# Performance work log

Measured on AMD Instinct MI355X. Metric: run time of the kernel, lower is better.

Reference implementation:

```python
import jax, jax.numpy as jnp
import numpy as np

N, E = 50000, 500000
DH, DL = 13, 128          # handcrafted / learned node feature dims
OH, OL = 32, 96           # node-encoder output dims; node_dim D = OH+OL
D = OH + OL               # 128
EIN = (DH + DL) + 1 + 3 * D + 1  # 527, forced by concat in forward
H = 256                   # MLP hidden width
HC = 64                   # classifier hidden width
EPS = 1e-8


def _mlp(x, W1, b1, W2, b2):
    # 2-layer MLP with ReLU, matching repo MLP(fc_dims=[H, out])
    return jax.nn.relu(x @ W1 + b1) @ W2 + b2


def _cosine(a, b):
    # torch.nn.CosineSimilarity(dim=1, eps=1e-8)
    na = jnp.maximum(jnp.linalg.norm(a, axis=-1), EPS)
    nb = jnp.maximum(jnp.linalg.norm(b, axis=-1), EPS)
    return jnp.sum(a * b, axis=-1) / (na * nb)


def _lin(key, fan_in, fan_out):
    kW, kb = jax.random.split(key)
    s = 1.0 / np.sqrt(fan_in)
    return (jax.random.uniform(kW, (fan_in, fan_out), jnp.float32, -s, s),
            jax.random.uniform(kb, (fan_out,), jnp.float32, -s, s))


def setup_inputs() -> dict:
    key = jax.random.key(0)
    ks = jax.random.split(key, 16)
    x1 = jax.random.normal(ks[0], (N, DH), jnp.float32)
    x2 = jax.random.normal(ks[1], (N, DL), jnp.float32)
    edge_index = jax.random.randint(ks[2], (2, E), 0, N, jnp.int64)
    Wh1, bh1 = _lin(ks[3], DH, H);   Wh2, bh2 = _lin(ks[4], H, OH)
    Wl1, bl1 = _lin(ks[5], DL, H);   Wl2, bl2 = _lin(ks[6], H, OL)
    We1, be1 = _lin(ks[7], EIN, H);  We2, be2 = _lin(ks[8], H, D)
    Wmsg, bmsg = _lin(ks[9], 2 * D, D)
    Wnode, bnode = _lin(ks[10], 2 * D, D)
    Wmp1, bmp1 = _lin(ks[11], 3 * D, H); Wmp2, bmp2 = _lin(ks[12], H, D)
    Wc1, bc1 = _lin(ks[13], D, HC);  Wc2, bc2 = _lin(ks[14], HC, 1)
    return dict(x1=x1, x2=x2, edge_index=edge_index,
                Wh1=Wh1, bh1=bh1, Wh2=Wh2, bh2=bh2,
                Wl1=Wl1, bl1=bl1, Wl2=Wl2, bl2=bl2,
                We1=We1, be1=be1, We2=We2, be2=be2,
                Wmsg=Wmsg, bmsg=bmsg, Wnode=Wnode, bnode=bnode,
                Wmp1=Wmp1, bmp1=bmp1, Wmp2=Wmp2, bmp2=bmp2,
                Wc1=Wc1, bc1=bc1, Wc2=Wc2, bc2=bc2)


def reference(x1, x2, edge_index,
              Wh1, bh1, Wh2, bh2,
              Wl1, bl1, Wl2, bl2,
              We1, be1, We2, be2,
              Wmsg, bmsg, Wnode, bnode,
              Wmp1, bmp1, Wmp2, bmp2,
              Wc1, bc1, Wc2, bc2):
    src, trg = edge_index[0], edge_index[1]
    # raw-feature edge descriptors
    x_init = jnp.concatenate((x1, x2), axis=-1)            # [N, 141]
    xi_s, xi_t = x_init[src], x_init[trg]                  # gathers [E, 141]
    sim1 = _cosine(xi_s, xi_t)                             # [E]
    abs_init = jnp.abs(xi_s - xi_t)                        # [E, 141]
    # node encoders
    h1 = _mlp(x1, Wh1, bh1, Wh2, bh2)                      # [N, 32]
    h2 = _mlp(x2, Wl1, bl1, Wl2, bl2)                      # [N, 96]
    x = jnp.concatenate((h1, h2), axis=-1)                 # [N, 128]
    xs, xt = x[src], x[trg]                                # [E, 128]
    sim2 = _cosine(xs, xt)                                 # [E]
    edge_feat_in = jnp.concatenate(
        (abs_init, sim1[:, None], xs, xt, jnp.abs(xs - xt), sim2[:, None]),
        axis=-1)                                           # [E, 527]
    e = _mlp(edge_feat_in, We1, be1, We2, be2)             # [E, 128]
    # edge MPNN round: edge->node aggregation, node update, edge update
    msg = jax.nn.relu(jnp.concatenate((xs, e), axis=-1) @ Wmsg + bmsg)  # [E, 128]
    agg = jax.ops.segment_sum(msg, trg, num_segments=N)    # [N, 128]
    xn = jax.nn.relu(jnp.concatenate((x, agg), axis=-1) @ Wnode + bnode)  # [N, 128]
    e_mp = _mlp(jnp.concatenate((xn[src], xn[trg], e), axis=-1),
                Wmp1, bmp1, Wmp2, bmp2)                    # [E, 128]
    pred = _mlp(e_mp, Wc1, bc1, Wc2, bc2)                  # [E, 1]
    return jnp.squeeze(pred, axis=-1)                      # [E]
```

## Files before the change

kernel.cpp:

```cpp
#include <hip/hip_runtime.h>
#include <hip/hip_bf16.h>
#include <hip/hip_fp16.h>


using fp16 = __half;
typedef _Float16 h16;
typedef _Float16 f16x8 __attribute__((ext_vector_type(8)));
typedef float f32x4 __attribute__((ext_vector_type(4)));

#define NN 50000
#define EE 500000
#define EPSC 1e-8f

__device__ __forceinline__ float reluf(float v){ return v > 0.f ? v : 0.f; }

#define OFF_E1   0
#define OFF_E2   139264
#define OFF_MSG  172032
#define OFF_NODE 204800
#define OFF_MP1  237568
#define OFF_MP2  335872
#define OFF_C1   368640
#define OFF_N1   376832
#define OFF_N2   458752
#define WT_TOTAL 524288
#define BF_TOTAL 640

__global__ __launch_bounds__(256) void k_prep(
    const float* __restrict__ We1, const float* __restrict__ We2,
    const float* __restrict__ Wmsg, const float* __restrict__ Wnode,
    const float* __restrict__ Wmp1, const float* __restrict__ Wmp2,
    const float* __restrict__ Wc1,
    const float* __restrict__ Wh1, const float* __restrict__ Wl1,
    const float* __restrict__ Wh2, const float* __restrict__ Wl2,
    const float* __restrict__ bh1, const float* __restrict__ bl1,
    const float* __restrict__ bh2, const float* __restrict__ bl2,
    h16* __restrict__ WT, float* __restrict__ BF)
{
  int idx = blockIdx.x * 256 + threadIdx.x;
  if (idx >= WT_TOTAL) {
    const int b = idx - WT_TOTAL;
    if (b < 512) BF[b] = (b < 256) ? bh1[b] : bl1[b - 256];
    else if (b < BF_TOTAL) {
      const int c = b - 512;
      BF[b] = (c < 32) ? bh2[c] : bl2[c - 32];
    }
    return;
  }
  h16 v;
  if (idx < OFF_E2) {
    const int L = idx, n = L / 544, k = L % 544;
    int r;
    if      (k < 128) r = 142 + k;
    else if (k < 256) r = 270 + (k - 128);
    else if (k < 384) r = 398 + (k - 256);
    else if (k < 512) r = 13 + (k - 384);
    else if (k < 525) r = k - 512;
    else if (k == 528) r = 141;
    else if (k == 529) r = 526;
    else r = -1;
    v = (h16)((r >= 0) ? We1[r * 256 + n] : 0.f);
  } else if (idx < OFF_MSG) {
    const int L = idx - OFF_E2, n = L >> 8, k = L & 255;
    v = (h16)We2[k * 128 + n];
  } else if (idx < OFF_NODE) {
    const int L = idx - OFF_MSG, n = L >> 8, k = L & 255;
    const int ko = (k < 128) ? (128 + k) : (k - 128);
    v = (h16)Wmsg[ko * 128 + n];
  } else if (idx < OFF_MP1) {
    const int L = idx - OFF_NODE, n = L >> 8, k = L & 255;
    v = (h16)Wnode[k * 128 + n];
  } else if (idx < OFF_MP2) {
    const int L = idx - OFF_MP1, n = L / 384, k = L % 384;
    v = (h16)Wmp1[k * 256 + n];
  } else if (idx < OFF_C1) {
    const int L = idx - OFF_MP2, n = L >> 8, k = L & 255;
    v = (h16)Wmp2[k * 128 + n];
  } else if (idx < OFF_N1) {
    const int L = idx - OFF_C1, n = L >> 7, k = L & 127;
    v = (h16)Wc1[k * 64 + n];
  } else if (idx < OFF_N2) {
    const int L = idx - OFF_N1, n = L / 160, k = L % 160;
    float f = 0.f;
    if (n < 256) { if (k < 13) f = Wh1[k * 256 + n]; }
    else { if (k >= 16 && k < 144) f = Wl1[(k - 16) * 256 + (n - 256)]; }
    v = (h16)f;
  } else {
    const int L = idx - OFF_N2, n = L >> 9, k = L & 511;
    float f = 0.f;
    if (n < 32) { if (k < 256) f = Wh2[k * 32 + n]; }
    else { if (k >= 256) f = Wl2[(k - 256) * 96 + (n - 32)]; }
    v = (h16)f;
  }
  WT[idx] = v;
}

__global__ __launch_bounds__(256) void k_cvt(
    const float* __restrict__ x1, const float* __restrict__ x2,
    h16* __restrict__ X1P, h16* __restrict__ X2H)
{
  const int idx = blockIdx.x * 256 + threadIdx.x;
  if (idx < NN * 16) {
    const int nn = idx >> 4, j = idx & 15;
    X1P[idx] = (h16)((j < 13) ? x1[nn * 13 + j] : 0.f);
  }
  const int i2 = idx - NN * 16;
  if (i2 >= 0 && i2 < NN * 128) X2H[i2] = (h16)x2[i2];
}

__global__ __launch_bounds__(256) void k_hist(
    const int* __restrict__ ei, int* __restrict__ CNT)
{
  const int e = blockIdx.x * 256 + threadIdx.x;
  if (e < EE) atomicAdd(&CNT[ei[EE + e]], 1);
}

__global__ __launch_bounds__(1024) void k_scan(
    const int* __restrict__ CNT, int* __restrict__ OFF)
{
  __shared__ int sdata[1024];
  __shared__ int scarry;
  const int tid = threadIdx.x;
  if (tid == 0) { scarry = 0; OFF[0] = 0; }
  __syncthreads();
  for (int base = 0; base < NN; base += 1024) {
    const int i = base + tid;
    sdata[tid] = (i < NN) ? CNT[i] : 0;
    __syncthreads();
    for (int off = 1; off < 1024; off <<= 1) {
      const int x = (tid >= off) ? sdata[tid - off] : 0;
      __syncthreads();
      sdata[tid] += x;
      __syncthreads();
    }
    const int carry = scarry;
    if (i < NN) OFF[i + 1] = sdata[tid] + carry;
    __syncthreads();
    if (tid == 0) scarry = carry + sdata[1023];
    __syncthreads();
  }
}

__global__ __launch_bounds__(256) void k_scatter(
    const int* __restrict__ ei, const int* __restrict__ OFF,
    int* __restrict__ POS, int* __restrict__ ES,
    int* __restrict__ ET, int* __restrict__ OID)
{
  const int e = blockIdx.x * 256 + threadIdx.x;
  if (e >= EE) return;
  const int t = ei[EE + e];
  const int p = atomicAdd(&POS[t], 1);
  const int idx = OFF[t] + p;
  ES[idx] = ei[e];
  ET[idx] = t;
  OID[idx] = e;
}

template<int ROWS, int UDIM, int KP, int LDA, int WAVES, bool RELU,
         bool ENDSYNC, typename F>
__device__ __forceinline__ void mfma_gemm(const h16* sA,
    const h16* __restrict__ WT, const float* __restrict__ bias, F emit)
{
  constexpr int RT = ROWS / 16;
  constexpr int NPW0 = UDIM / WAVES;
  constexpr int NPW = (NPW0 < 16) ? 16 : NPW0;
  constexpr int NT = NPW / 16;
  constexpr int NSTEPS = KP / 32;
  constexpr int CH0 = (NT >= 4) ? 2 : 4;
  constexpr int CHUNK = (NSTEPS < CH0) ? NSTEPS : CH0;
  constexpr int NCH = (NSTEPS + CHUNK - 1) / CHUNK;
  const int tid = threadIdx.x;
  const int wave = tid >> 6;
  const int lane = tid & 63;
  const int m = lane & 15;
  const int quad = lane >> 4;
  const int n0 = wave * NPW;
  const bool active = (n0 < UDIM);

  f32x4 acc[RT][NT];
#pragma unroll
  for (int r = 0; r < RT; ++r)
#pragma unroll
    for (int j = 0; j < NT; ++j) acc[r][j] = (f32x4){0.f, 0.f, 0.f, 0.f};
  float bb[NT];

  if (active) {
    const h16* wbase = &WT[(size_t)(n0 + m) * KP + quad * 8];
#pragma unroll
    for (int j = 0; j < NT; ++j) bb[j] = bias[n0 + j * 16 + m];

    f16x8 breg[2][CHUNK][NT];
#pragma unroll
    for (int s = 0; s < CHUNK; ++s)
      if (s < NSTEPS)
#pragma unroll
        for (int j = 0; j < NT; ++j)
          breg[0][s][j] = *(const f16x8*)&wbase[(size_t)j * 16 * KP + s * 32];
    asm volatile("" ::: "memory");

#pragma unroll
    for (int c = 0; c < NCH; ++c) {
      if (c + 1 < NCH) {
#pragma unroll
        for (int s = 0; s < CHUNK; ++s) {
          const int st = (c + 1) * CHUNK + s;
          if (st < NSTEPS)
#pragma unroll
            for (int j = 0; j < NT; ++j)
              breg[(c + 1) & 1][s][j] =
                  *(const f16x8*)&wbase[(size_t)j * 16 * KP + st * 32];
        }
      }
#pragma unroll
      for (int s = 0; s < CHUNK; ++s) {
        const int st = c * CHUNK + s;
        if (st < NSTEPS) {
          const int k0 = st * 32;
#pragma unroll
          for (int r = 0; r < RT; ++r) {
            const f16x8 af = *(const f16x8*)&sA[(r * 16 + m) * LDA + k0 + quad * 8];
#pragma unroll
            for (int j = 0; j < NT; ++j)
              acc[r][j] = __builtin_amdgcn_mfma_f32_16x16x32_f16(af, breg[c & 1][s][j], acc[r][j], 0, 0, 0);
          }
        }
      }
      asm volatile("" ::: "memory");
    }
  }
  __syncthreads();
  if (active) {
#pragma unroll
    for (int j = 0; j < NT; ++j) {
      const int col = n0 + j * 16 + m;
#pragma unroll
      for (int r = 0; r < RT; ++r)
#pragma unroll
        for (int g = 0; g < 4; ++g) {
          const int row = r * 16 + quad * 4 + g;
          float v = acc[r][j][g] + bb[j];
          if (RELU) v = reluf(v);
          emit(row, col, v);
        }
    }
  }
  if (ENDSYNC) __syncthreads();
}

__global__ __launch_bounds__(512, 4) void k_nenc(
    const h16* __restrict__ X1P, const h16* __restrict__ X2H,
    const h16* __restrict__ WT, const float* __restrict__ BF,
    h16* __restrict__ XH)
{
  __shared__ __align__(16) h16 sA[32 * 168];
  __shared__ __align__(16) h16 sH[32 * 520];
  const int tid = threadIdx.x;
  const int n0 = blockIdx.x * 32;
  const int remn = NN - n0;
  const int cnt = remn < 32 ? remn : 32;
  const int n = tid >> 4;
  const int q = tid & 15;

  if (n < cnt) {
    const int node = n0 + n;
    if (q < 2)
      *(f16x8*)&sA[n * 168 + q * 8] = *(const f16x8*)&X1P[node * 16 + q * 8];
    else if (q < 4)
      *(f16x8*)&sA[n * 168 + 144 + (q - 2) * 8] = (f16x8){};
    *(f16x8*)&sA[n * 168 + 16 + q * 8] =
        *(const f16x8*)&X2H[(size_t)node * 128 + q * 8];
  }
  __syncthreads();

  mfma_gemm<32, 512, 160, 168, 8, true, true>(sA, WT + OFF_N1, BF,
      [&](int row, int col, float v) { sH[row * 520 + col] = (h16)v; });
  mfma_gemm<32, 128, 512, 520, 8, false, false>(sH, WT + OFF_N2, BF + 512,
      [&](int row, int col, float v) {
        if (row < cnt) XH[(size_t)(n0 + row) * 128 + col] = (h16)v;
      });
}

__global__ __launch_bounds__(512, 4) void k_edge_mlp(
    const h16* __restrict__ X1P, const h16* __restrict__ X2H,
    const int* __restrict__ ES, const int* __restrict__ ET,
    const h16* __restrict__ XH, const h16* __restrict__ WT,
    const float* __restrict__ be1, const float* __restrict__ be2,
    const float* __restrict__ bmsg,
    h16* __restrict__ EB, float* __restrict__ AGG)
{
  __shared__ __align__(16) h16 sFeat[64 * 568];
  __shared__ int strg[64];
  const int tid = threadIdx.x;
  const long e0 = (long)blockIdx.x * 64;
  const long rem = (long)EE - e0;
  const int cnt = rem < 64 ? (int)rem : 64;
  const int n = tid >> 3;
  const int q = tid & 7;
  h16* Arow = &sFeat[n * 568];
  f16x8 xsv0 = {}, xsv1 = {};

  if (n < cnt) {
    const int s = ES[e0 + n];
    const int t = ET[e0 + n];
    if (q == 0) strg[n] = t;
    float ds = 0.f, ns = 0.f, nt = 0.f;
    if (q < 2) {
      const f16x8 a = *(const f16x8*)&X1P[s * 16 + q * 8];
      const f16x8 b = *(const f16x8*)&X1P[t * 16 + q * 8];
      f16x8 d;
#pragma unroll
      for (int i = 0; i < 8; ++i) {
        const float av = (float)a[i], bv = (float)b[i];
        ds += av * bv; ns += av * av; nt += bv * bv;
        d[i] = (h16)fabsf(av - bv);
      }
      *(f16x8*)&Arow[512 + q * 8] = d;
    }
#pragma unroll
    for (int c = 0; c < 2; ++c) {
      const f16x8 a = *(const f16x8*)&X2H[(size_t)s * 128 + q * 16 + c * 8];
      const f16x8 b = *(const f16x8*)&X2H[(size_t)t * 128 + q * 16 + c * 8];
      f16x8 d;
#pragma unroll
      for (int i = 0; i < 8; ++i) {
        const float av = (float)a[i], bv = (float)b[i];
        ds += av * bv; ns += av * av; nt += bv * bv;
        d[i] = (h16)fabsf(av - bv);
      }
      *(f16x8*)&Arow[384 + q * 16 + c * 8] = d;
    }
    ds += __shfl_xor(ds, 1); ds += __shfl_xor(ds, 2); ds += __shfl_xor(ds, 4);
    ns += __shfl_xor(ns, 1); ns += __shfl_xor(ns, 2); ns += __shfl_xor(ns, 4);
    nt += __shfl_xor(nt, 1); nt += __shfl_xor(nt, 2); nt += __shfl_xor(nt, 4);
    if (q == 0)
      Arow[528] = (h16)(ds / (fmaxf(sqrtf(ns), EPSC) * fmaxf(sqrtf(nt), EPSC)));

    float ds2 = 0.f, ns2 = 0.f, nt2 = 0.f;
#pragma unroll
    for (int c = 0; c < 2; ++c) {
      const f16x8 a = *(const f16x8*)&XH[(size_t)s * 128 + q * 16 + c * 8];
      const f16x8 b = *(const f16x8*)&XH[(size_t)t * 128 + q * 16 + c * 8];
      if (c == 0) xsv0 = a; else xsv1 = a;
      f16x8 d;
#pragma unroll
      for (int i = 0; i < 8; ++i) {
        const float av = (float)a[i], bv = (float)b[i];
        ds2 += av * bv; ns2 += av * av; nt2 += bv * bv;
        d[i] = (h16)fabsf(av - bv);
      }
      *(f16x8*)&Arow[q * 16 + c * 8]       = a;
      *(f16x8*)&Arow[128 + q * 16 + c * 8] = b;
      *(f16x8*)&Arow[256 + q * 16 + c * 8] = d;
    }
    ds2 += __shfl_xor(ds2, 1); ds2 += __shfl_xor(ds2, 2); ds2 += __shfl_xor(ds2, 4);
    ns2 += __shfl_xor(ns2, 1); ns2 += __shfl_xor(ns2, 2); ns2 += __shfl_xor(ns2, 4);
    nt2 += __shfl_xor(nt2, 1); nt2 += __shfl_xor(nt2, 2); nt2 += __shfl_xor(nt2, 4);
    if (q == 0)
      Arow[529] = (h16)(ds2 / (fmaxf(sqrtf(ns2), EPSC) * fmaxf(sqrtf(nt2), EPSC)));
    for (int j = 530 + q; j < 544; j += 8) Arow[j] = (h16)0.f;
  } else {
    if (q == 0) strg[n] = 0;
    for (int j8 = q; j8 < 71; j8 += 8) *(f16x8*)&Arow[j8 * 8] = (f16x8){};
  }
  __syncthreads();

  h16* sHid = sFeat;
  mfma_gemm<64, 256, 544, 568, 8, true, true>(sFeat, WT + OFF_E1, be1,
      [&](int row, int col, float v) { sHid[row * 264 + col] = (h16)v; });
  mfma_gemm<64, 128, 256, 264, 8, false, false>(sHid, WT + OFF_E2, be2,
      [&](int row, int col, float v) {
        const h16 vh = (h16)v;
        if (row < cnt) EB[(size_t)(e0 + row) * 128 + col] = vh;
        sHid[row * 264 + col] = vh;
      });
  *(f16x8*)&sFeat[n * 264 + 128 + q * 16]     = xsv0;
  *(f16x8*)&sFeat[n * 264 + 128 + q * 16 + 8] = xsv1;
  __syncthreads();
  mfma_gemm<64, 128, 256, 264, 8, true, true>(sFeat, WT + OFF_MSG, bmsg,
      [&](int row, int col, float v) {
        *(float*)((char*)sFeat + row * 528 + col * 4) = v;
      });
  {
    const int c = tid & 127;
    const int g = tid >> 7;
    const int r0 = g * 16;
    if (r0 < cnt) {
      const int rend = (r0 + 16 < cnt) ? r0 + 16 : cnt;
      float acc = 0.f;
      int cur = strg[r0];
      for (int r = r0; r < rend; ++r) {
        const int t = strg[r];
        if (t != cur) {
          atomicAdd(&AGG[(size_t)cur * 128 + c], acc);
          acc = 0.f; cur = t;
        }
        acc += *(const float*)((const char*)sFeat + r * 528 + c * 4);
      }
      atomicAdd(&AGG[(size_t)cur * 128 + c], acc);
    }
  }
}

__global__ __launch_bounds__(256, 4) void k_node_update(
    const h16* __restrict__ XH, const float* __restrict__ AGG,
    const h16* __restrict__ WT, const float* __restrict__ bnode,
    h16* __restrict__ XNH)
{
  __shared__ __align__(16) h16 sA[64 * 264];
  const int tid = threadIdx.x;
  const int n0 = blockIdx.x * 64;
  const int remn = NN - n0;
  const int cnt = remn < 64 ? remn : 64;
  const int n = tid >> 2;
  const int q = tid & 3;

  if (n < cnt) {
    const f16x8* xr = (const f16x8*)&XH[(size_t)(n0 + n) * 128];
    const float4* ar = (const float4*)&AGG[(size_t)(n0 + n) * 128];
    for (int j8 = q; j8 < 16; j8 += 4)
      *(f16x8*)&sA[n * 264 + j8 * 8] = xr[j8];
    for (int j4 = q; j4 < 32; j4 += 4) {
      const float4 b = ar[j4];
      h16* p1 = &sA[n * 264 + 128 + j4 * 4];
      p1[0] = (h16)b.x; p1[1] = (h16)b.y; p1[2] = (h16)b.z; p1[3] = (h16)b.w;
    }
  } else {
    for (int j = q; j < 256; j += 4) sA[n * 264 + j] = (h16)0.f;
  }
  __syncthreads();

  mfma_gemm<64, 128, 256, 264, 4, true, false>(sA, WT + OFF_NODE, bnode,
      [&](int row, int col, float v) {
        if (row < cnt) XNH[(size_t)(n0 + row) * 128 + col] = (h16)v;
      });
}

__global__ __launch_bounds__(512, 4) void k_empl(
    const int* __restrict__ ES, const int* __restrict__ ET,
    const int* __restrict__ OID, const h16* __restrict__ XNH,
    const h16* __restrict__ EB, const h16* __restrict__ WT,
    const float* __restrict__ bmp1, const float* __restrict__ bmp2,
    const float* __restrict__ bc1,
    const float* __restrict__ Wc2, const float* __restrict__ bc2,
    float* __restrict__ out)
{
  __shared__ __align__(16) h16 sF[64 * 392];
  const int tid = threadIdx.x;
  const long e0 = (long)blockIdx.x * 64;
  const long rem = (long)EE - e0;
  const int cnt = rem < 64 ? (int)rem : 64;
  const int n = tid >> 3;
  const int q = tid & 7;

  if (n < cnt) {
    const int s = ES[e0 + n];
    const int t = ET[e0 + n];
    const f16x8* xsr = (const f16x8*)&XNH[(size_t)s * 128];
    const f16x8* xtr = (const f16x8*)&XNH[(size_t)t * 128];
    const f16x8* ebr = (const f16x8*)&EB[(size_t)(e0 + n) * 128];
#pragma unroll
    for (int j8 = q; j8 < 16; j8 += 8) {
      *(f16x8*)&sF[n * 392 + j8 * 8]       = xsr[j8];
      *(f16x8*)&sF[n * 392 + 128 + j8 * 8] = xtr[j8];
      *(f16x8*)&sF[n * 392 + 256 + j8 * 8] = ebr[j8];
    }
  } else {
    for (int j8 = q; j8 < 49; j8 += 8) *(f16x8*)&sF[n * 392 + j8 * 8] = (f16x8){};
  }
  __syncthreads();

  h16*  sH2 = sF;
  h16*  sE  = sF;
  float* sHC = (float*)((char*)sF + 17408);
  mfma_gemm<64, 256, 384, 392, 8, true, true>(sF, WT + OFF_MP1, bmp1,
      [&](int row, int col, float v) { sH2[row * 264 + col] = (h16)v; });
  mfma_gemm<64, 128, 256, 264, 8, false, true>(sH2, WT + OFF_MP2, bmp2,
      [&](int row, int col, float v) { sE[row * 136 + col] = (h16)v; });
  mfma_gemm<64, 64, 128, 136, 8, true, true>(sE, WT + OFF_C1, bc1,
      [&](int row, int col, float v) { sHC[row * 65 + col] = v; });
  if (tid < cnt) {
    float acc = bc2[0];
    for (int k = 0; k < 64; ++k) acc += sHC[tid * 65 + k] * Wc2[k];
    out[OID[e0 + tid]] = acc;
  }
}

extern "C" void kernel_launch(void* const* d_in, const int* in_sizes, int n_in,
                              void* d_out, int out_size, void* d_ws, size_t ws_size,
                              hipStream_t stream)
{
  const float* x1  = (const float*)d_in[0];
  const float* x2  = (const float*)d_in[1];
  const int*   ei  = (const int*)d_in[2];
  const float* Wh1 = (const float*)d_in[3],  *bh1 = (const float*)d_in[4];
  const float* Wh2 = (const float*)d_in[5],  *bh2 = (const float*)d_in[6];
  const float* Wl1 = (const float*)d_in[7],  *bl1 = (const float*)d_in[8];
  const float* Wl2 = (const float*)d_in[9],  *bl2 = (const float*)d_in[10];
  const float* We1 = (const float*)d_in[11], *be1 = (const float*)d_in[12];
  const float* We2 = (const float*)d_in[13], *be2 = (const float*)d_in[14];
  const float* Wmsg = (const float*)d_in[15], *bmsg = (const float*)d_in[16];
  const float* Wnode = (const float*)d_in[17], *bnode = (const float*)d_in[18];
  const float* Wmp1 = (const float*)d_in[19], *bmp1 = (const float*)d_in[20];
  const float* Wmp2 = (const float*)d_in[21], *bmp2 = (const float*)d_in[22];
  const float* Wc1 = (const float*)d_in[23], *bc1 = (const float*)d_in[24];
  const float* Wc2 = (const float*)d_in[25], *bc2 = (const float*)d_in[26];
  float* out = (float*)d_out;

  float* AGG = (float*)d_ws;
  h16*   EB  = (h16*)(AGG + (size_t)NN * 128);
  h16*   WT  = EB + (size_t)EE * 128;
  h16*   XH  = WT + WT_TOTAL;
  h16*   XNH = XH + (size_t)NN * 128;
  h16*   X1P = XNH + (size_t)NN * 128;
  h16*   X2H = X1P + (size_t)NN * 16;
  float* BF  = (float*)(X2H + (size_t)NN * 128);
  int*   CNT = (int*)(BF + BF_TOTAL);
  int*   POS = CNT + NN;
  int*   OFF = POS + NN;
  int*   ES  = OFF + (NN + 1);
  int*   ET  = ES + EE;
  int*   OID = ET + EE;

  k_prep<<<(WT_TOTAL + BF_TOTAL + 255) / 256, 256, 0, stream>>>(
      We1, We2, Wmsg, Wnode, Wmp1, Wmp2, Wc1,
      Wh1, Wl1, Wh2, Wl2, bh1, bl1, bh2, bl2, WT, BF);
  k_cvt<<<(NN * 16 + NN * 128 + 255) / 256, 256, 0, stream>>>(x1, x2, X1P, X2H);
  hipMemsetAsync(AGG, 0, (size_t)NN * 128 * sizeof(float), stream);
  hipMemsetAsync(CNT, 0, (size_t)2 * NN * sizeof(int), stream);
  k_hist<<<(EE + 255) / 256, 256, 0, stream>>>(ei, CNT);
  k_scan<<<1, 1024, 0, stream>>>(CNT, OFF);
  k_scatter<<<(EE + 255) / 256, 256, 0, stream>>>(ei, OFF, POS, ES, ET, OID);
  k_nenc<<<(NN + 31) / 32, 512, 0, stream>>>(X1P, X2H, WT, BF, XH);
  k_edge_mlp<<<7813, 512, 0, stream>>>(X1P, X2H, ES, ET, XH, WT,
                                       be1, be2, bmsg, EB, AGG);
  k_node_update<<<782, 256, 0, stream>>>(XH, AGG, WT, bnode, XNH);
  k_empl<<<7813, 512, 0, stream>>>(ES, ET, OID, XNH, EB, WT, bmp1, bmp2, bc1,
                                   Wc2, bc2, out);
}
```

Before: 951.3 us.

## Parallelize CSR scan, fuse histogram into convert, use fdot2 for cosine features

Replaces the single-block serial prefix scan over 50k node counts with a two-level multi-block scan, so this step is no longer a one-workgroup bottleneck. The in-degree histogram is folded into the input-conversion kernel to save a launch. The edge-feature kernel now computes its dot products and norms with packed fp16 dot2 instructions and takes absolute differences with a sign-bit mask, reducing per-element conversion work. The dot products now take fp16 inputs with fp32 accumulation, and the absolute differences are computed in fp16 rather than fp32, which may change rounding slightly.

```diff
diff --git a/kernel.cpp b/kernel.cpp
--- a/kernel.cpp
+++ b/kernel.cpp
@@ -6,13 +6,35 @@
 using fp16 = __half;
 typedef _Float16 h16;
 typedef _Float16 f16x8 __attribute__((ext_vector_type(8)));
+typedef _Float16 h16x2 __attribute__((ext_vector_type(2)));
+typedef short s16x8 __attribute__((ext_vector_type(8)));
 typedef float f32x4 __attribute__((ext_vector_type(4)));
 
 #define NN 50000
 #define EE 500000
 #define EPSC 1e-8f
+#define SCAN_B 196
 
 __device__ __forceinline__ float reluf(float v){ return v > 0.f ? v : 0.f; }
+
+__device__ __forceinline__ float dot8(const f16x8 a, const f16x8 b, float acc)
+{
+#pragma unroll
+  for (int i = 0; i < 4; ++i) {
+    const h16x2 av = {a[2 * i], a[2 * i + 1]};
+    const h16x2 bv = {b[2 * i], b[2 * i + 1]};
+    acc = __builtin_amdgcn_fdot2(av, bv, acc, false);
+  }
+  return acc;
+}
+
+__device__ __forceinline__ f16x8 absdiff8(const f16x8 a, const f16x8 b)
+{
+  const f16x8 d = a - b;
+  s16x8 di = __builtin_bit_cast(s16x8, d);
+  di &= (short)0x7fff;
+  return __builtin_bit_cast(f16x8, di);
+}
 
 #define OFF_E1   0
 #define OFF_E2   139264
@@ -97,9 +119,11 @@
 
 __global__ __launch_bounds__(256) void k_cvt(
     const float* __restrict__ x1, const float* __restrict__ x2,
-    h16* __restrict__ X1P, h16* __restrict__ X2H)
+    const int* __restrict__ ei,
+    h16* __restrict__ X1P, h16* __restrict__ X2H, int* __restrict__ CNT)
 {
   const int idx = blockIdx.x * 256 + threadIdx.x;
+  if (idx < EE) atomicAdd(&CNT[ei[EE + idx]], 1);
   if (idx < NN * 16) {
     const int nn = idx >> 4, j = idx & 15;
     X1P[idx] = (h16)((j < 13) ? x1[nn * 13 + j] : 0.f);
@@ -108,49 +132,52 @@
   if (i2 >= 0 && i2 < NN * 128) X2H[i2] = (h16)x2[i2];
 }
 
-__global__ __launch_bounds__(256) void k_hist(
-    const int* __restrict__ ei, int* __restrict__ CNT)
-{
-  const int e = blockIdx.x * 256 + threadIdx.x;
-  if (e < EE) atomicAdd(&CNT[ei[EE + e]], 1);
-}
-
-__global__ __launch_bounds__(1024) void k_scan(
-    const int* __restrict__ CNT, int* __restrict__ OFF)
-{
-  __shared__ int sdata[1024];
-  __shared__ int scarry;
-  const int tid = threadIdx.x;
-  if (tid == 0) { scarry = 0; OFF[0] = 0; }
-  __syncthreads();
-  for (int base = 0; base < NN; base += 1024) {
-    const int i = base + tid;
-    sdata[tid] = (i < NN) ? CNT[i] : 0;
+__global__ __launch_bounds__(256) void k_scanA(
+    const int* __restrict__ CNT, int* __restrict__ TEX, int* __restrict__ BS)
+{
+  __shared__ int sd[256];
+  const int tid = threadIdx.x;
+  const int i = blockIdx.x * 256 + tid;
+  const int v = (i < NN) ? CNT[i] : 0;
+  sd[tid] = v;
+  __syncthreads();
+  for (int off = 1; off < 256; off <<= 1) {
+    const int x = (tid >= off) ? sd[tid - off] : 0;
     __syncthreads();
-    for (int off = 1; off < 1024; off <<= 1) {
-      const int x = (tid >= off) ? sdata[tid - off] : 0;
-      __syncthreads();
-      sdata[tid] += x;
-      __syncthreads();
-    }
-    const int carry = scarry;
-    if (i < NN) OFF[i + 1] = sdata[tid] + carry;
+    sd[tid] += x;
     __syncthreads();
-    if (tid == 0) scarry = carry + sdata[1023];
+  }
+  if (i < NN) TEX[i] = sd[tid] - v;
+  if (tid == 255) BS[blockIdx.x] = sd[255];
+}
+
+__global__ __launch_bounds__(256) void k_scanB(
+    const int* __restrict__ BS, int* __restrict__ BSSE)
+{
+  __shared__ int sd[256];
+  const int tid = threadIdx.x;
+  const int v = (tid < SCAN_B) ? BS[tid] : 0;
+  sd[tid] = v;
+  __syncthreads();
+  for (int off = 1; off < 256; off <<= 1) {
+    const int x = (tid >= off) ? sd[tid - off] : 0;
     __syncthreads();
-  }
+    sd[tid] += x;
+    __syncthreads();
+  }
+  if (tid < SCAN_B) BSSE[tid] = sd[tid] - v;
 }
 
 __global__ __launch_bounds__(256) void k_scatter(
-    const int* __restrict__ ei, const int* __restrict__ OFF,
-    int* __restrict__ POS, int* __restrict__ ES,
-    int* __restrict__ ET, int* __restrict__ OID)
+    const int* __restrict__ ei, const int* __restrict__ TEX,
+    const int* __restrict__ BSSE, int* __restrict__ POS,
+    int* __restrict__ ES, int* __restrict__ ET, int* __restrict__ OID)
 {
   const int e = blockIdx.x * 256 + threadIdx.x;
   if (e >= EE) return;
   const int t = ei[EE + e];
   const int p = atomicAdd(&POS[t], 1);
-  const int idx = OFF[t] + p;
+  const int idx = BSSE[t >> 8] + TEX[t] + p;
   ES[idx] = ei[e];
   ET[idx] = t;
   OID[idx] = e;
@@ -307,27 +334,15 @@
     if (q < 2) {
       const f16x8 a = *(const f16x8*)&X1P[s * 16 + q * 8];
       const f16x8 b = *(const f16x8*)&X1P[t * 16 + q * 8];
-      f16x8 d;
-#pragma unroll
-      for (int i = 0; i < 8; ++i) {
-        const float av = (float)a[i], bv = (float)b[i];
-        ds += av * bv; ns += av * av; nt += bv * bv;
-        d[i] = (h16)fabsf(av - bv);
-      }
-      *(f16x8*)&Arow[512 + q * 8] = d;
+      ds = dot8(a, b, ds); ns = dot8(a, a, ns); nt = dot8(b, b, nt);
+      *(f16x8*)&Arow[512 + q * 8] = absdiff8(a, b);
     }
 #pragma unroll
     for (int c = 0; c < 2; ++c) {
       const f16x8 a = *(const f16x8*)&X2H[(size_t)s * 128 + q * 16 + c * 8];
       const f16x8 b = *(const f16x8*)&X2H[(size_t)t * 128 + q * 16 + c * 8];
-      f16x8 d;
-#pragma unroll
-      for (int i = 0; i < 8; ++i) {
-        const float av = (float)a[i], bv = (float)b[i];
-        ds += av * bv; ns += av * av; nt += bv * bv;
-        d[i] = (h16)fabsf(av - bv);
-      }
-      *(f16x8*)&Arow[384 + q * 16 + c * 8] = d;
+      ds = dot8(a, b, ds); ns = dot8(a, a, ns); nt = dot8(b, b, nt);
+      *(f16x8*)&Arow[384 + q * 16 + c * 8] = absdiff8(a, b);
     }
     ds += __shfl_xor(ds, 1); ds += __shfl_xor(ds, 2); ds += __shfl_xor(ds, 4);
     ns += __shfl_xor(ns, 1); ns += __shfl_xor(ns, 2); ns += __shfl_xor(ns, 4);
@@ -341,16 +356,10 @@
       const f16x8 a = *(const f16x8*)&XH[(size_t)s * 128 + q * 16 + c * 8];
       const f16x8 b = *(const f16x8*)&XH[(size_t)t * 128 + q * 16 + c * 8];
       if (c == 0) xsv0 = a; else xsv1 = a;
-      f16x8 d;
-#pragma unroll
-      for (int i = 0; i < 8; ++i) {
-        const float av = (float)a[i], bv = (float)b[i];
-        ds2 += av * bv; ns2 += av * av; nt2 += bv * bv;
-        d[i] = (h16)fabsf(av - bv);
-      }
+      ds2 = dot8(a, b, ds2); ns2 = dot8(a, a, ns2); nt2 = dot8(b, b, nt2);
       *(f16x8*)&Arow[q * 16 + c * 8]       = a;
       *(f16x8*)&Arow[128 + q * 16 + c * 8] = b;
-      *(f16x8*)&Arow[256 + q * 16 + c * 8] = d;
+      *(f16x8*)&Arow[256 + q * 16 + c * 8] = absdiff8(a, b);
     }
     ds2 += __shfl_xor(ds2, 1); ds2 += __shfl_xor(ds2, 2); ds2 += __shfl_xor(ds2, 4);
     ns2 += __shfl_xor(ns2, 1); ns2 += __shfl_xor(ns2, 2); ns2 += __shfl_xor(ns2, 4);
@@ -516,20 +525,23 @@
   float* BF  = (float*)(X2H + (size_t)NN * 128);
   int*   CNT = (int*)(BF + BF_TOTAL);
   int*   POS = CNT + NN;
-  int*   OFF = POS + NN;
-  int*   ES  = OFF + (NN + 1);
+  int*   TEX = POS + NN;
+  int*   ES  = TEX + NN;
   int*   ET  = ES + EE;
   int*   OID = ET + EE;
+  int*   BS  = OID + EE;
+  int*   BSSE = BS + 256;
 
   k_prep<<<(WT_TOTAL + BF_TOTAL + 255) / 256, 256, 0, stream>>>(
       We1, We2, Wmsg, Wnode, Wmp1, Wmp2, Wc1,
       Wh1, Wl1, Wh2, Wl2, bh1, bl1, bh2, bl2, WT, BF);
-  k_cvt<<<(NN * 16 + NN * 128 + 255) / 256, 256, 0, stream>>>(x1, x2, X1P, X2H);
   hipMemsetAsync(AGG, 0, (size_t)NN * 128 * sizeof(float), stream);
   hipMemsetAsync(CNT, 0, (size_t)2 * NN * sizeof(int), stream);
-  k_hist<<<(EE + 255) / 256, 256, 0, stream>>>(ei, CNT);
-  k_scan<<<1, 1024, 0, stream>>>(CNT, OFF);
-  k_scatter<<<(EE + 255) / 256, 256, 0, stream>>>(ei, OFF, POS, ES, ET, OID);
+  k_cvt<<<(NN * 16 + NN * 128 + 255) / 256, 256, 0, stream>>>(
+      x1, x2, ei, X1P, X2H, CNT);
+  k_scanA<<<SCAN_B, 256, 0, stream>>>(CNT, TEX, BS);
+  k_scanB<<<1, 256, 0, stream>>>(BS, BSSE);
+  k_scatter<<<(EE + 255) / 256, 256, 0, stream>>>(ei, TEX, BSSE, POS, ES, ET, OID);
   k_nenc<<<(NN + 31) / 32, 512, 0, stream>>>(X1P, X2H, WT, BF, XH);
   k_edge_mlp<<<7813, 512, 0, stream>>>(X1P, X2H, ES, ET, XH, WT,
                                        be1, be2, bmsg, EB, AGG);
```

New measurement: 867.4 us. 8.8% less time.
